# Optimization experiments

Hardware: AMD Instinct MI355X
Metric: run time of the kernel (lower is better)

Reference implementation:

```python
import jax, jax.numpy as jnp
import numpy as np

N_NODES = 100000
N_EDGES = 1600000
F_IN = 128
F_OUT = 32
HEADS = 8
ALPHA = 0.2  # LeakyReLU slope


def setup_inputs() -> dict:
    key = jax.random.key(0)
    ks = jax.random.split(key, 7)
    x = jax.random.normal(ks[0], (N_NODES, F_IN), dtype=jnp.float32)
    row = jnp.sort(jax.random.randint(ks[1], (N_EDGES,), 0, N_NODES, dtype=jnp.int32))
    col = jax.random.randint(ks[2], (N_EDGES,), 0, N_NODES, dtype=jnp.int32)
    kernels = jax.random.normal(ks[3], (HEADS, F_IN, F_OUT), dtype=jnp.float32) * 0.1
    att_self = jax.random.normal(ks[4], (HEADS, F_OUT), dtype=jnp.float32) * 0.1
    att_neigh = jax.random.normal(ks[5], (HEADS, F_OUT), dtype=jnp.float32) * 0.1
    biases = jax.random.normal(ks[6], (HEADS, F_OUT), dtype=jnp.float32) * 0.1
    return {"x": x, "row": row, "col": col, "kernels": kernels,
            "att_self": att_self, "att_neigh": att_neigh, "biases": biases}


def reference(x, row, col, kernels, att_self, att_neigh, biases):
    # GraphAttention (GAT), eval mode (dropout inactive), concat over heads.
    N = x.shape[0]
    outs = []
    for h in range(kernels.shape[0]):  # fixed small head loop
        feat = x @ kernels[h]                     # [N, F_OUT]
        a_s = feat @ att_self[h]                  # [N]
        a_n = feat @ att_neigh[h]                 # [N]
        e = a_s[row] + a_n[col]                   # [E] edge logits (SDDMM)
        e = jnp.where(e > 0, e, ALPHA * e)        # LeakyReLU(0.2)
        # row-wise (destination-node) sparse softmax, numerically stable
        m = jax.ops.segment_max(e, row, num_segments=N)
        ex = jnp.exp(e - m[row])
        denom = jax.ops.segment_sum(ex, row, num_segments=N)
        alpha = ex / denom[row]                   # [E]
        # SpMM: out[i] = sum_{e: row[e]=i} alpha[e] * feat[col[e]]
        msg = alpha[:, None] * feat[col]          # [E, F_OUT]
        out = jax.ops.segment_sum(msg, row, num_segments=N) + biases[h]
        outs.append(out)
    return jnp.concatenate(outs, axis=1)          # [N, HEADS*F_OUT]
```

## Files before the change

### kernel.cpp

```cpp
#include <hip/hip_runtime.h>
#include <hip/hip_bf16.h>
#include <math.h>


#define F_IN   128
#define F_ALL  256
#define HEADS  8
#define F_OUT  32
#define ALPHA  0.2f
#define CHUNK  128

__global__ __launch_bounds__(256) void feat_gemm(const float* __restrict__ x,
                                                 const float* __restrict__ kern,
                                                 const float* __restrict__ att_s,
                                                 const float* __restrict__ att_n,
                                                 __hip_bfloat16* __restrict__ featb,
                                                 float* __restrict__ a_s,
                                                 float* __restrict__ a_n, int N) {
  __shared__ float As[32][64];
  __shared__ float Bs[32][256];
  const int t  = threadIdx.x;
  const int tx = t & 31, ty = t >> 5;
  const int n0 = blockIdx.x * 64;
  const int r0 = ty * 8, c0 = tx * 8;

  float acc[8][8];
#pragma unroll
  for (int i = 0; i < 8; i++)
#pragma unroll
    for (int j = 0; j < 8; j++) acc[i][j] = 0.f;

  const float4* kern4 = reinterpret_cast<const float4*>(kern);

  for (int kc = 0; kc < F_IN; kc += 32) {
    __syncthreads();
#pragma unroll
    for (int rep = 0; rep < 2; ++rep) {
      int v = t + rep * 256;
      int n = v >> 3, k4 = v & 7;
      int nn = n0 + n; if (nn >= N) nn = N - 1;
      float4 xv = *reinterpret_cast<const float4*>(&x[(size_t)nn * F_IN + kc + k4 * 4]);
      As[k4 * 4 + 0][n] = xv.x;
      As[k4 * 4 + 1][n] = xv.y;
      As[k4 * 4 + 2][n] = xv.z;
      As[k4 * 4 + 3][n] = xv.w;
    }
#pragma unroll
    for (int rep = 0; rep < 8; ++rep) {
      int v = t + rep * 256;
      int k = v >> 6, rem = v & 63;
      int h = rem >> 3, f4 = rem & 7;
      float4 wv = kern4[((size_t)h * F_IN + kc + k) * 8 + f4];
      *reinterpret_cast<float4*>(&Bs[k][rem * 4]) = wv;
    }
    __syncthreads();
#pragma unroll
    for (int k = 0; k < 32; ++k) {
      float4 a0 = *reinterpret_cast<const float4*>(&As[k][r0]);
      float4 a1 = *reinterpret_cast<const float4*>(&As[k][r0 + 4]);
      float4 b0 = *reinterpret_cast<const float4*>(&Bs[k][c0]);
      float4 b1 = *reinterpret_cast<const float4*>(&Bs[k][c0 + 4]);
      float av[8] = {a0.x, a0.y, a0.z, a0.w, a1.x, a1.y, a1.z, a1.w};
      float bv[8] = {b0.x, b0.y, b0.z, b0.w, b1.x, b1.y, b1.z, b1.w};
#pragma unroll
      for (int i = 0; i < 8; i++)
#pragma unroll
        for (int j = 0; j < 8; j++) acc[i][j] = fmaf(av[i], bv[j], acc[i][j]);
    }
  }

  const int h  = tx >> 2;
  const int jb = (tx & 3) * 8;
  float sv[8], nv[8];
#pragma unroll
  for (int j = 0; j < 8; j++) {
    sv[j] = att_s[h * F_OUT + jb + j];
    nv[j] = att_n[h * F_OUT + jb + j];
  }
#pragma unroll
  for (int i = 0; i < 8; i++) {
    int n = n0 + r0 + i;
    if (n < N) {
      alignas(16) __hip_bfloat16 hb[8];
#pragma unroll
      for (int j = 0; j < 8; j++) hb[j] = __float2bfloat16(acc[i][j]);
      *reinterpret_cast<float4*>(&featb[(size_t)n * F_ALL + c0]) =
          *reinterpret_cast<const float4*>(hb);
      float ps = 0.f, pn = 0.f;
#pragma unroll
      for (int j = 0; j < 8; j++) {
        ps = fmaf(acc[i][j], sv[j], ps);
        pn = fmaf(acc[i][j], nv[j], pn);
      }
      ps += __shfl_xor(ps, 1); ps += __shfl_xor(ps, 2);
      pn += __shfl_xor(pn, 1); pn += __shfl_xor(pn, 2);
      if ((tx & 3) == 0) {
        a_s[n * HEADS + h] = ps;
        a_n[n * HEADS + h] = pn;
      }
    }
  }
}

__global__ __launch_bounds__(256) void row_ptr_k(const int* __restrict__ row,
                                                 int* __restrict__ ptr, int N, int E) {
  int n = blockIdx.x * 256 + threadIdx.x;
  if (n > N) return;
  int lo = 0, hi = E;
  while (lo < hi) {
    int mid = (lo + hi) >> 1;
    if (row[mid] < n) lo = mid + 1; else hi = mid;
  }
  ptr[n] = lo;
}

__global__ __launch_bounds__(256) void gat_scatter(const __hip_bfloat16* __restrict__ featb,
                                                   const float* __restrict__ a_s,
                                                   const float* __restrict__ a_n,
                                                   const int* __restrict__ col,
                                                   const int* __restrict__ ptr,
                                                   const float* __restrict__ biases,
                                                   float* __restrict__ out, int N) {
  __shared__ float wlds[HEADS][CHUNK + 1];
  __shared__ int   clds[CHUNK];
  const int n = blockIdx.x;
  const int t = threadIdx.x;
  const int h = t >> 5;
  const int f = t & 31;
  const int start = ptr[n], end = ptr[n + 1];
  const int deg = end - start;
  const float as = a_s[n * HEADS + h];

  float mx = -INFINITY;
  for (int e = f; e < deg; e += 32) {
    int c = col[start + e];
    float ev = as + a_n[c * HEADS + h];
    ev = ev > 0.f ? ev : ALPHA * ev;
    mx = fmaxf(mx, ev);
    if (e < CHUNK) {
      wlds[h][e] = ev;
      if (h == 0) clds[e] = c;
    }
  }
#pragma unroll
  for (int m = 16; m; m >>= 1) mx = fmaxf(mx, __shfl_xor(mx, m));

  float sm = 0.f;
  for (int e = f; e < deg; e += 32) {
    float ev;
    if (e < CHUNK) ev = wlds[h][e];
    else {
      int c = col[start + e];
      ev = as + a_n[c * HEADS + h];
      ev = ev > 0.f ? ev : ALPHA * ev;
    }
    float ex = __expf(ev - mx);
    sm += ex;
    if (e < CHUNK) wlds[h][e] = ex;
  }
#pragma unroll
  for (int m = 16; m; m >>= 1) sm += __shfl_xor(sm, m);
  const float inv = (deg > 0) ? 1.0f / sm : 0.0f;

  __syncthreads();

  float ac0 = 0.f, ac1 = 0.f, ac2 = 0.f, ac3 = 0.f;
  const int base = h * F_OUT + f;
  {
    const int cn = deg < CHUNK ? deg : CHUNK;
    int e = 0;
    for (; e + 4 <= cn; e += 4) {
      int ca = clds[e], cb = clds[e + 1], cc = clds[e + 2], cd = clds[e + 3];
      float wa = wlds[h][e],     wb = wlds[h][e + 1];
      float wc = wlds[h][e + 2], wd = wlds[h][e + 3];
      float fa = __bfloat162float(featb[(size_t)ca * F_ALL + base]);
      float fb = __bfloat162float(featb[(size_t)cb * F_ALL + base]);
      float fc = __bfloat162float(featb[(size_t)cc * F_ALL + base]);
      float fd = __bfloat162float(featb[(size_t)cd * F_ALL + base]);
      ac0 = fmaf(wa, fa, ac0);
      ac1 = fmaf(wb, fb, ac1);
      ac2 = fmaf(wc, fc, ac2);
      ac3 = fmaf(wd, fd, ac3);
    }
    for (; e < cn; ++e)
      ac0 = fmaf(wlds[h][e], __bfloat162float(featb[(size_t)clds[e] * F_ALL + base]), ac0);
  }

  for (int cs = CHUNK; cs < deg; cs += CHUNK) {
    __syncthreads();
    int cn = deg - cs; if (cn > CHUNK) cn = CHUNK;
    for (int e = f; e < cn; e += 32) {
      int c = col[start + cs + e];
      if (h == 0) clds[e] = c;
      float ev = as + a_n[c * HEADS + h];
      ev = ev > 0.f ? ev : ALPHA * ev;
      wlds[h][e] = __expf(ev - mx);
    }
    __syncthreads();
    int e = 0;
    for (; e + 4 <= cn; e += 4) {
      int ca = clds[e], cb = clds[e + 1], cc = clds[e + 2], cd = clds[e + 3];
      float wa = wlds[h][e],     wb = wlds[h][e + 1];
      float wc = wlds[h][e + 2], wd = wlds[h][e + 3];
      ac0 = fmaf(wa, __bfloat162float(featb[(size_t)ca * F_ALL + base]), ac0);
      ac1 = fmaf(wb, __bfloat162float(featb[(size_t)cb * F_ALL + base]), ac1);
      ac2 = fmaf(wc, __bfloat162float(featb[(size_t)cc * F_ALL + base]), ac2);
      ac3 = fmaf(wd, __bfloat162float(featb[(size_t)cd * F_ALL + base]), ac3);
    }
    for (; e < cn; ++e)
      ac0 = fmaf(wlds[h][e], __bfloat162float(featb[(size_t)clds[e] * F_ALL + base]), ac0);
  }

  out[(size_t)n * F_ALL + t] = (ac0 + ac1 + ac2 + ac3) * inv + biases[t];
}

extern "C" void kernel_launch(void* const* d_in, const int* in_sizes, int n_in,
                              void* d_out, int out_size, void* d_ws, size_t ws_size,
                              hipStream_t stream) {
  const float* x      = (const float*)d_in[0];
  const int*   row    = (const int*)d_in[1];
  const int*   col    = (const int*)d_in[2];
  const float* kern   = (const float*)d_in[3];
  const float* att_s  = (const float*)d_in[4];
  const float* att_n  = (const float*)d_in[5];
  const float* biases = (const float*)d_in[6];

  const int N = in_sizes[0] / F_IN;
  const int E = in_sizes[1];

  __hip_bfloat16* featb = (__hip_bfloat16*)d_ws;
  float* a_s = (float*)(featb + (size_t)N * F_ALL);
  float* a_n = a_s + (size_t)N * HEADS;
  int*   ptr = (int*)(a_n + (size_t)N * HEADS);
  float* out = (float*)d_out;

  hipLaunchKernelGGL(feat_gemm, dim3((N + 63) / 64), dim3(256), 0, stream,
                     x, kern, att_s, att_n, featb, a_s, a_n, N);
  hipLaunchKernelGGL(row_ptr_k, dim3((N + 1 + 255) / 256), dim3(256), 0, stream, row, ptr, N, E);
  hipLaunchKernelGGL(gat_scatter, dim3(N), dim3(256), 0, stream,
                     featb, a_s, a_n, col, ptr, biases, out, N);
}
```

Baseline: 316.5 us.

## Use bf16 MFMA for feature GEMM, fold attention projections, add low-degree scatter path

Replaces the fp32 SIMT feature GEMM with a bf16 MFMA kernel fed by a prep kernel that converts x and transposes the weights to bf16. The attention logits are now computed directly from x using precomputed kernel·att vectors in a separate a_proj kernel. gat_scatter gains a fast path for nodes with degree ≤32 that keeps edge weights in registers, exchanges them with shuffles and reads packed bf16 pairs, and returns early for zero-degree nodes. This adds two extra launches and an extra pass over x, and the a_s/a_n logits are now computed from fp32 x instead of the fp32 GEMM output.

```diff
diff --git a/kernel.cpp b/kernel.cpp
--- a/kernel.cpp
+++ b/kernel.cpp
@@ -10,94 +10,121 @@
 #define ALPHA  0.2f
 #define CHUNK  128
 
-__global__ __launch_bounds__(256) void feat_gemm(const float* __restrict__ x,
-                                                 const float* __restrict__ kern,
-                                                 const float* __restrict__ att_s,
-                                                 const float* __restrict__ att_n,
-                                                 __hip_bfloat16* __restrict__ featb,
-                                                 float* __restrict__ a_s,
-                                                 float* __restrict__ a_n, int N) {
-  __shared__ float As[32][64];
-  __shared__ float Bs[32][256];
+using f32x4  = __attribute__((ext_vector_type(4))) float;
+using bf16x8 = __attribute__((ext_vector_type(8))) short;
+using u16x8  = __attribute__((ext_vector_type(8))) unsigned short;
+
+static __device__ __forceinline__ unsigned short f32_to_bf16(float f) {
+  union { float f; unsigned u; } v; v.f = f;
+  unsigned r = v.u + 0x7FFF + ((v.u >> 16) & 1);
+  return (unsigned short)(r >> 16);
+}
+static __device__ __forceinline__ float bf16_lo(unsigned d) {
+  return __uint_as_float(d << 16);
+}
+static __device__ __forceinline__ float bf16_hi(unsigned d) {
+  return __uint_as_float(d & 0xffff0000u);
+}
+
+__global__ __launch_bounds__(256) void prep(const float* __restrict__ x,
+                                            const float* __restrict__ kern,
+                                            const float* __restrict__ att_s,
+                                            const float* __restrict__ att_n,
+                                            unsigned short* __restrict__ xb,
+                                            unsigned short* __restrict__ Wt,
+                                            float* __restrict__ ws,
+                                            float* __restrict__ wn,
+                                            int total_x8) {
+  int id = blockIdx.x * 256 + threadIdx.x;
+  if (id < total_x8) {
+    const float4* x4 = reinterpret_cast<const float4*>(x);
+    float4 v0 = x4[(size_t)id * 2], v1 = x4[(size_t)id * 2 + 1];
+    u16x8 o;
+    o[0] = f32_to_bf16(v0.x); o[1] = f32_to_bf16(v0.y);
+    o[2] = f32_to_bf16(v0.z); o[3] = f32_to_bf16(v0.w);
+    o[4] = f32_to_bf16(v1.x); o[5] = f32_to_bf16(v1.y);
+    o[6] = f32_to_bf16(v1.z); o[7] = f32_to_bf16(v1.w);
+    *reinterpret_cast<u16x8*>(xb + (size_t)id * 8) = o;
+  }
+  if (id < F_ALL * F_IN) {
+    int c = id >> 7, k = id & 127;
+    Wt[id] = f32_to_bf16(kern[(size_t)(c >> 5) * (F_IN * F_OUT) + k * F_OUT + (c & 31)]);
+  }
+  if (id < 2 * HEADS * F_IN) {
+    int which = id >> 10;
+    int hk = id & 1023;
+    int h = hk >> 7, k = hk & 127;
+    const float* att = which ? att_n : att_s;
+    float s = 0.f;
+#pragma unroll
+    for (int f = 0; f < F_OUT; ++f)
+      s += kern[(size_t)h * (F_IN * F_OUT) + k * F_OUT + f] * att[h * F_OUT + f];
+    (which ? wn : ws)[hk] = s;
+  }
+}
+
+__global__ __launch_bounds__(256) void a_proj(const float* __restrict__ x,
+                                              const float* __restrict__ ws,
+                                              const float* __restrict__ wn,
+                                              float* __restrict__ a_s,
+                                              float* __restrict__ a_n, int NH) {
+  int id = blockIdx.x * 256 + threadIdx.x;
+  if (id >= NH) return;
+  int n = id >> 3, h = id & 7;
+  const float4* xr = reinterpret_cast<const float4*>(x) + (size_t)n * 32;
+  const float4* sr = reinterpret_cast<const float4*>(ws) + h * 32;
+  const float4* nr = reinterpret_cast<const float4*>(wn) + h * 32;
+  float ss = 0.f, sn = 0.f;
+#pragma unroll 8
+  for (int i = 0; i < 32; ++i) {
+    float4 xv = xr[i], sv = sr[i], nv = nr[i];
+    ss += xv.x * sv.x + xv.y * sv.y + xv.z * sv.z + xv.w * sv.w;
+    sn += xv.x * nv.x + xv.y * nv.y + xv.z * nv.z + xv.w * nv.w;
+  }
+  a_s[id] = ss;
+  a_n[id] = sn;
+}
+
+__global__ __launch_bounds__(256) void feat_gemm_mfma(
+    const unsigned short* __restrict__ xb,
+    const unsigned short* __restrict__ Wt,
+    unsigned short* __restrict__ featb,
+    int N) {
   const int t  = threadIdx.x;
-  const int tx = t & 31, ty = t >> 5;
-  const int n0 = blockIdx.x * 64;
-  const int r0 = ty * 8, c0 = tx * 8;
-
-  float acc[8][8];
-#pragma unroll
-  for (int i = 0; i < 8; i++)
-#pragma unroll
-    for (int j = 0; j < 8; j++) acc[i][j] = 0.f;
-
-  const float4* kern4 = reinterpret_cast<const float4*>(kern);
-
-  for (int kc = 0; kc < F_IN; kc += 32) {
-    __syncthreads();
-#pragma unroll
-    for (int rep = 0; rep < 2; ++rep) {
-      int v = t + rep * 256;
-      int n = v >> 3, k4 = v & 7;
-      int nn = n0 + n; if (nn >= N) nn = N - 1;
-      float4 xv = *reinterpret_cast<const float4*>(&x[(size_t)nn * F_IN + kc + k4 * 4]);
-      As[k4 * 4 + 0][n] = xv.x;
-      As[k4 * 4 + 1][n] = xv.y;
-      As[k4 * 4 + 2][n] = xv.z;
-      As[k4 * 4 + 3][n] = xv.w;
-    }
-#pragma unroll
-    for (int rep = 0; rep < 8; ++rep) {
-      int v = t + rep * 256;
-      int k = v >> 6, rem = v & 63;
-      int h = rem >> 3, f4 = rem & 7;
-      float4 wv = kern4[((size_t)h * F_IN + kc + k) * 8 + f4];
-      *reinterpret_cast<float4*>(&Bs[k][rem * 4]) = wv;
-    }
-    __syncthreads();
-#pragma unroll
-    for (int k = 0; k < 32; ++k) {
-      float4 a0 = *reinterpret_cast<const float4*>(&As[k][r0]);
-      float4 a1 = *reinterpret_cast<const float4*>(&As[k][r0 + 4]);
-      float4 b0 = *reinterpret_cast<const float4*>(&Bs[k][c0]);
-      float4 b1 = *reinterpret_cast<const float4*>(&Bs[k][c0 + 4]);
-      float av[8] = {a0.x, a0.y, a0.z, a0.w, a1.x, a1.y, a1.z, a1.w};
-      float bv[8] = {b0.x, b0.y, b0.z, b0.w, b1.x, b1.y, b1.z, b1.w};
-#pragma unroll
-      for (int i = 0; i < 8; i++)
-#pragma unroll
-        for (int j = 0; j < 8; j++) acc[i][j] = fmaf(av[i], bv[j], acc[i][j]);
-    }
-  }
-
-  const int h  = tx >> 2;
-  const int jb = (tx & 3) * 8;
-  float sv[8], nv[8];
-#pragma unroll
-  for (int j = 0; j < 8; j++) {
-    sv[j] = att_s[h * F_OUT + jb + j];
-    nv[j] = att_n[h * F_OUT + jb + j];
-  }
-#pragma unroll
-  for (int i = 0; i < 8; i++) {
-    int n = n0 + r0 + i;
+  const int w  = t >> 6;
+  const int l  = t & 63;
+  const int lr = l & 15;
+  const int lq = l >> 4;
+  const int n0 = blockIdx.x * 64 + w * 16;
+
+  f32x4 acc[16];
+#pragma unroll
+  for (int ct = 0; ct < 16; ++ct) acc[ct] = (f32x4){0.f, 0.f, 0.f, 0.f};
+
+  int ar = n0 + lr; if (ar >= N) ar = N - 1;
+  const unsigned short* xrow = xb + (size_t)ar * F_IN + lq * 8;
+  bf16x8 afr[4];
+#pragma unroll
+  for (int kc = 0; kc < 4; ++kc)
+    afr[kc] = *reinterpret_cast<const bf16x8*>(xrow + kc * 32);
+
+#pragma unroll
+  for (int ct = 0; ct < 16; ++ct) {
+    const unsigned short* wrow = Wt + (size_t)(ct * 16 + lr) * F_IN + lq * 8;
+#pragma unroll
+    for (int kc = 0; kc < 4; ++kc) {
+      bf16x8 bfr = *reinterpret_cast<const bf16x8*>(wrow + kc * 32);
+      acc[ct] = __builtin_amdgcn_mfma_f32_16x16x32_bf16(afr[kc], bfr, acc[ct], 0, 0, 0);
+    }
+  }
+
+#pragma unroll
+  for (int r = 0; r < 4; ++r) {
+    int n = n0 + lq * 4 + r;
     if (n < N) {
-      alignas(16) __hip_bfloat16 hb[8];
-#pragma unroll
-      for (int j = 0; j < 8; j++) hb[j] = __float2bfloat16(acc[i][j]);
-      *reinterpret_cast<float4*>(&featb[(size_t)n * F_ALL + c0]) =
-          *reinterpret_cast<const float4*>(hb);
-      float ps = 0.f, pn = 0.f;
-#pragma unroll
-      for (int j = 0; j < 8; j++) {
-        ps = fmaf(acc[i][j], sv[j], ps);
-        pn = fmaf(acc[i][j], nv[j], pn);
-      }
-      ps += __shfl_xor(ps, 1); ps += __shfl_xor(ps, 2);
-      pn += __shfl_xor(pn, 1); pn += __shfl_xor(pn, 2);
-      if ((tx & 3) == 0) {
-        a_s[n * HEADS + h] = ps;
-        a_n[n * HEADS + h] = pn;
-      }
+#pragma unroll
+      for (int ct = 0; ct < 16; ++ct)
+        featb[(size_t)n * F_ALL + ct * 16 + lr] = f32_to_bf16(acc[ct][r]);
     }
   }
 }
@@ -114,32 +141,88 @@
   ptr[n] = lo;
 }
 
-__global__ __launch_bounds__(256) void gat_scatter(const __hip_bfloat16* __restrict__ featb,
-                                                   const float* __restrict__ a_s,
-                                                   const float* __restrict__ a_n,
-                                                   const int* __restrict__ col,
-                                                   const int* __restrict__ ptr,
-                                                   const float* __restrict__ biases,
-                                                   float* __restrict__ out, int N) {
+__global__ __launch_bounds__(256) void gat_scatter(
+    const unsigned short* __restrict__ featb,
+    const float* __restrict__ a_s, const float* __restrict__ a_n,
+    const int* __restrict__ col, const int* __restrict__ ptr,
+    const float* __restrict__ biases, float* __restrict__ out, int N) {
   __shared__ float wlds[HEADS][CHUNK + 1];
   __shared__ int   clds[CHUNK];
   const int n = blockIdx.x;
   const int t = threadIdx.x;
   const int h = t >> 5;
   const int f = t & 31;
-  const int start = ptr[n], end = ptr[n + 1];
-  const int deg = end - start;
+  const int start = ptr[n];
+  const int deg   = ptr[n + 1] - start;
+
+  if (deg == 0) { out[(size_t)n * F_ALL + t] = biases[t]; return; }
   const float as = a_s[n * HEADS + h];
+  const unsigned* fu32 = reinterpret_cast<const unsigned*>(featb);
+
+  if (deg <= 32) {
+    int c = 0; float ev = -INFINITY;
+    if (f < deg) {
+      c = col[start + f];
+      float e0 = as + a_n[c * HEADS + h];
+      ev = e0 > 0.f ? e0 : ALPHA * e0;
+    }
+    float mx = ev;
+#pragma unroll
+    for (int m = 16; m; m >>= 1) mx = fmaxf(mx, __shfl_xor(mx, m));
+    float ex = (f < deg) ? __expf(ev - mx) : 0.f;
+    float sm = ex;
+#pragma unroll
+    for (int m = 16; m; m >>= 1) sm += __shfl_xor(sm, m);
+    const float inv = 1.0f / sm;
+
+    const int q = f & 15, p = f >> 4;
+    const int dbase = h * 16 + q;
+    float a0 = 0.f, a1 = 0.f, b0 = 0.f, b1 = 0.f;
+    int e = 0;
+    for (; e + 4 <= deg; e += 4) {
+      int   ca = __shfl(c,  e + p,     32);
+      float wa = __shfl(ex, e + p,     32);
+      int   cb = __shfl(c,  e + 2 + p, 32);
+      float wb = __shfl(ex, e + 2 + p, 32);
+      unsigned da = fu32[ca * 128 + dbase];
+      unsigned db = fu32[cb * 128 + dbase];
+      a0 = fmaf(wa, bf16_lo(da), a0);
+      a1 = fmaf(wa, bf16_hi(da), a1);
+      b0 = fmaf(wb, bf16_lo(db), b0);
+      b1 = fmaf(wb, bf16_hi(db), b1);
+    }
+    for (; e < deg; e += 2) {
+      int idx = e + p;
+      int cl  = idx < deg ? idx : 0;
+      int   ca = __shfl(c,  cl, 32);
+      float wa = __shfl(ex, cl, 32);
+      if (idx >= deg) wa = 0.f;
+      unsigned da = fu32[ca * 128 + dbase];
+      a0 = fmaf(wa, bf16_lo(da), a0);
+      a1 = fmaf(wa, bf16_hi(da), a1);
+    }
+    a0 += b0; a1 += b1;
+    a0 += __shfl_xor(a0, 16);
+    a1 += __shfl_xor(a1, 16);
+    if (p == 0) {
+      const float2 bv = *reinterpret_cast<const float2*>(&biases[h * F_OUT + q * 2]);
+      float2 o;
+      o.x = a0 * inv + bv.x;
+      o.y = a1 * inv + bv.y;
+      *reinterpret_cast<float2*>(&out[(size_t)n * F_ALL + h * F_OUT + q * 2]) = o;
+    }
+    return;
+  }
 
   float mx = -INFINITY;
   for (int e = f; e < deg; e += 32) {
-    int c = col[start + e];
-    float ev = as + a_n[c * HEADS + h];
-    ev = ev > 0.f ? ev : ALPHA * ev;
-    mx = fmaxf(mx, ev);
+    int cc = col[start + e];
+    float e0 = as + a_n[cc * HEADS + h];
+    e0 = e0 > 0.f ? e0 : ALPHA * e0;
+    mx = fmaxf(mx, e0);
     if (e < CHUNK) {
-      wlds[h][e] = ev;
-      if (h == 0) clds[e] = c;
+      wlds[h][e] = e0;
+      if (h == 0) clds[e] = cc;
     }
   }
 #pragma unroll
@@ -147,20 +230,20 @@
 
   float sm = 0.f;
   for (int e = f; e < deg; e += 32) {
-    float ev;
-    if (e < CHUNK) ev = wlds[h][e];
+    float e0;
+    if (e < CHUNK) e0 = wlds[h][e];
     else {
-      int c = col[start + e];
-      ev = as + a_n[c * HEADS + h];
-      ev = ev > 0.f ? ev : ALPHA * ev;
-    }
-    float ex = __expf(ev - mx);
-    sm += ex;
-    if (e < CHUNK) wlds[h][e] = ex;
+      int cc = col[start + e];
+      e0 = as + a_n[cc * HEADS + h];
+      e0 = e0 > 0.f ? e0 : ALPHA * e0;
+    }
+    float x2 = __expf(e0 - mx);
+    sm += x2;
+    if (e < CHUNK) wlds[h][e] = x2;
   }
 #pragma unroll
   for (int m = 16; m; m >>= 1) sm += __shfl_xor(sm, m);
-  const float inv = (deg > 0) ? 1.0f / sm : 0.0f;
+  const float inv = 1.0f / sm;
 
   __syncthreads();
 
@@ -173,44 +256,30 @@
       int ca = clds[e], cb = clds[e + 1], cc = clds[e + 2], cd = clds[e + 3];
       float wa = wlds[h][e],     wb = wlds[h][e + 1];
       float wc = wlds[h][e + 2], wd = wlds[h][e + 3];
-      float fa = __bfloat162float(featb[(size_t)ca * F_ALL + base]);
-      float fb = __bfloat162float(featb[(size_t)cb * F_ALL + base]);
-      float fc = __bfloat162float(featb[(size_t)cc * F_ALL + base]);
-      float fd = __bfloat162float(featb[(size_t)cd * F_ALL + base]);
-      ac0 = fmaf(wa, fa, ac0);
-      ac1 = fmaf(wb, fb, ac1);
-      ac2 = fmaf(wc, fc, ac2);
-      ac3 = fmaf(wd, fd, ac3);
+      ac0 = fmaf(wa, __uint_as_float((unsigned)featb[(size_t)ca * F_ALL + base] << 16), ac0);
+      ac1 = fmaf(wb, __uint_as_float((unsigned)featb[(size_t)cb * F_ALL + base] << 16), ac1);
+      ac2 = fmaf(wc, __uint_as_float((unsigned)featb[(size_t)cc * F_ALL + base] << 16), ac2);
+      ac3 = fmaf(wd, __uint_as_float((unsigned)featb[(size_t)cd * F_ALL + base] << 16), ac3);
     }
     for (; e < cn; ++e)
-      ac0 = fmaf(wlds[h][e], __bfloat162float(featb[(size_t)clds[e] * F_ALL + base]), ac0);
-  }
-
+      ac0 = fmaf(wlds[h][e],
+                 __uint_as_float((unsigned)featb[(size_t)clds[e] * F_ALL + base] << 16), ac0);
+  }
   for (int cs = CHUNK; cs < deg; cs += CHUNK) {
     __syncthreads();
     int cn = deg - cs; if (cn > CHUNK) cn = CHUNK;
     for (int e = f; e < cn; e += 32) {
-      int c = col[start + cs + e];
-      if (h == 0) clds[e] = c;
-      float ev = as + a_n[c * HEADS + h];
-      ev = ev > 0.f ? ev : ALPHA * ev;
-      wlds[h][e] = __expf(ev - mx);
+      int cc = col[start + cs + e];
+      if (h == 0) clds[e] = cc;
+      float e0 = as + a_n[cc * HEADS + h];
+      e0 = e0 > 0.f ? e0 : ALPHA * e0;
+      wlds[h][e] = __expf(e0 - mx);
     }
     __syncthreads();
-    int e = 0;
-    for (; e + 4 <= cn; e += 4) {
-      int ca = clds[e], cb = clds[e + 1], cc = clds[e + 2], cd = clds[e + 3];
-      float wa = wlds[h][e],     wb = wlds[h][e + 1];
-      float wc = wlds[h][e + 2], wd = wlds[h][e + 3];
-      ac0 = fmaf(wa, __bfloat162float(featb[(size_t)ca * F_ALL + base]), ac0);
-      ac1 = fmaf(wb, __bfloat162float(featb[(size_t)cb * F_ALL + base]), ac1);
-      ac2 = fmaf(wc, __bfloat162float(featb[(size_t)cc * F_ALL + base]), ac2);
-      ac3 = fmaf(wd, __bfloat162float(featb[(size_t)cd * F_ALL + base]), ac3);
-    }
-    for (; e < cn; ++e)
-      ac0 = fmaf(wlds[h][e], __bfloat162float(featb[(size_t)clds[e] * F_ALL + base]), ac0);
-  }
-
+    for (int e = 0; e < cn; ++e)
+      ac0 = fmaf(wlds[h][e],
+                 __uint_as_float((unsigned)featb[(size_t)clds[e] * F_ALL + base] << 16), ac0);
+  }
   out[(size_t)n * F_ALL + t] = (ac0 + ac1 + ac2 + ac3) * inv + biases[t];
 }
 
@@ -228,14 +297,23 @@
   const int N = in_sizes[0] / F_IN;
   const int E = in_sizes[1];
 
-  __hip_bfloat16* featb = (__hip_bfloat16*)d_ws;
-  float* a_s = (float*)(featb + (size_t)N * F_ALL);
+  unsigned short* featb = (unsigned short*)d_ws;
+  unsigned short* xb    = featb + (size_t)N * F_ALL;
+  unsigned short* Wt    = xb + (size_t)N * F_IN;
+  float* ws  = (float*)(Wt + F_ALL * F_IN);
+  float* wn  = ws + HEADS * F_IN;
+  float* a_s = wn + HEADS * F_IN;
   float* a_n = a_s + (size_t)N * HEADS;
   int*   ptr = (int*)(a_n + (size_t)N * HEADS);
   float* out = (float*)d_out;
 
-  hipLaunchKernelGGL(feat_gemm, dim3((N + 63) / 64), dim3(256), 0, stream,
-                     x, kern, att_s, att_n, featb, a_s, a_n, N);
+  const int total_x8 = N * F_IN / 8;
+  hipLaunchKernelGGL(prep, dim3((total_x8 + 255) / 256), dim3(256), 0, stream,
+                     x, kern, att_s, att_n, xb, Wt, ws, wn, total_x8);
+  hipLaunchKernelGGL(a_proj, dim3((N * HEADS + 255) / 256), dim3(256), 0, stream,
+                     x, ws, wn, a_s, a_n, N * HEADS);
+  hipLaunchKernelGGL(feat_gemm_mfma, dim3((N + 63) / 64), dim3(256), 0, stream,
+                     xb, Wt, featb, N);
   hipLaunchKernelGGL(row_ptr_k, dim3((N + 1 + 255) / 256), dim3(256), 0, stream, row, ptr, N, E);
   hipLaunchKernelGGL(gat_scatter, dim3(N), dim3(256), 0, stream,
                      featb, a_s, a_n, col, ptr, biases, out, N);
```

New measurement: 390.2 us. 1.23x slower.
